# Optimization experiments

Measured on AMD Instinct MI355X. Metric: run time of the kernel, lower is better.

## Reference

```python
import jax, jax.numpy as jnp
import numpy as np

B, T, HID = 2, 1024, 4096
H, D_NOPE, D_ROPE, D_V = 32, 128, 64, 128
D_QK = D_NOPE + D_ROPE  # 192
Q_RANK, KV_RANK = 1536, 512
THETA, EPS = 10000.0, 1e-6
SCALE = D_QK ** -0.5
NEG = -1e30


def rms_norm(x, w):
    return x * jax.lax.rsqrt(jnp.mean(x * x, axis=-1, keepdims=True) + EPS) * w


def apply_rope(x, positions):
    # x: [B, T, h, d] (d even), positions: [B, T]
    d = x.shape[-1]
    inv_freq = 1.0 / (THETA ** (jnp.arange(0, d, 2, dtype=jnp.float32) / d))
    ang = positions.astype(jnp.float32)[:, :, None, None] * inv_freq  # [B,T,1,d/2]
    cos, sin = jnp.cos(ang), jnp.sin(ang)
    x1, x2 = jnp.split(x, 2, axis=-1)
    return jnp.concatenate([x1 * cos - x2 * sin, x1 * sin + x2 * cos], axis=-1)


def setup_inputs() -> dict:
    key = jax.random.key(0)
    ks = jax.random.split(key, 8)
    def lin(k, fan_in, fan_out):
        return (jax.random.normal(k, (fan_in, fan_out), jnp.float32)
                / np.float32(np.sqrt(fan_in)))
    return {
        "x": jax.random.normal(ks[0], (B, T, HID), jnp.float32),
        "wq_a": lin(ks[1], HID, Q_RANK),
        "q_norm_w": jnp.ones((Q_RANK,), jnp.float32),
        "wq_b": lin(ks[2], Q_RANK, H * D_QK),
        "wkv_a": lin(ks[3], HID, KV_RANK + D_ROPE),
        "kv_norm_w": jnp.ones((KV_RANK,), jnp.float32),
        "wkv_b": lin(ks[4], KV_RANK, H * (D_NOPE + D_V)),
        "wo": lin(ks[5], H * D_V, HID),
        "attention_mask": jnp.ones((B, T), jnp.int32),
        "positions": jnp.broadcast_to(jnp.arange(T, dtype=jnp.int32), (B, T)),
    }


def reference(x, wq_a, q_norm_w, wq_b, wkv_a, kv_norm_w, wkv_b, wo,
              attention_mask, positions):
    # ---- query path: low-rank down-proj, RMSNorm, up-proj ----
    q = rms_norm(x @ wq_a, q_norm_w) @ wq_b           # [B,T,H*D_QK]
    q = q.reshape(B, T, H, D_QK)
    q_nope, q_pe = jnp.split(q, [D_NOPE], axis=-1)
    q_pe = apply_rope(q_pe, positions)                # [B,T,H,D_ROPE]

    # ---- kv path: compressed latent + shared rope key ----
    kv_out = x @ wkv_a                                # [B,T,KV_RANK+D_ROPE]
    kv, k_pe = jnp.split(kv_out, [KV_RANK], axis=-1)
    k_pe = apply_rope(k_pe[:, :, None, :], positions) # [B,T,1,D_ROPE]
    kv_exp = rms_norm(kv, kv_norm_w) @ wkv_b          # [B,T,H*(D_NOPE+D_V)]
    kv_exp = kv_exp.reshape(B, T, H, D_NOPE + D_V)
    k_nope, v = jnp.split(kv_exp, [D_NOPE], axis=-1)

    q = jnp.concatenate([q_nope, q_pe], axis=-1)      # [B,T,H,D_QK]
    k = jnp.concatenate(
        [k_nope, jnp.broadcast_to(k_pe, (B, T, H, D_ROPE))], axis=-1)

    # ---- attention (causal + padding mask) ----
    scores = jnp.einsum('bthd,bshd->bhts', q, k) * SCALE     # [B,H,T,T]
    causal = jnp.tril(jnp.ones((T, T), dtype=bool))
    mask = causal[None, None] & (attention_mask[:, None, None, :] != 0)
    scores = jnp.where(mask, scores, NEG)
    attn = jax.nn.softmax(scores, axis=-1)
    out = jnp.einsum('bhts,bshd->bthd', attn, v)              # [B,T,H,D_V]
    return out.reshape(B, T, H * D_V) @ wo                    # [B,T,HID]
```

## Files before the change

kernel.cpp:

```cpp
#include <hip/hip_runtime.h>
#include <hip/hip_bf16.h>

#define BB 2
#define TT 1024
#define HIDD 4096
#define NH 32
#define DN 128
#define DR 64
#define DVV 128
#define DQK 192
#define QR 1536
#define KVR 512
#define MTOK (BB*TT)
#define EPSF 1e-6f
#define SCALEF 0.07216878364870322f

typedef unsigned short u16;
using bfrag = __attribute__((ext_vector_type(8))) short;
using f4 = __attribute__((ext_vector_type(4))) float;

__device__ __forceinline__ float bf2f(u16 u){
    union { unsigned int i; float f; } v; v.i = ((unsigned int)u) << 16; return v.f;
}
__device__ __forceinline__ u16 f2bf(float f){
    union { float f; unsigned int i; } v; v.f = f;
    unsigned int r = v.i + 0x7fffu + ((v.i >> 16) & 1u);
    return (u16)(r >> 16);
}
__device__ __forceinline__ void async16(const void* g, void* l){
    __builtin_amdgcn_global_load_lds((const __attribute__((address_space(1))) void*)g,
                                     (__attribute__((address_space(3))) void*)l, 16, 0, 0);
}

__global__ __launch_bounds__(256) void cvt_k(const float* __restrict__ in,
                                             u16* __restrict__ out, int n)
{
    int i = (blockIdx.x * 256 + threadIdx.x) * 4;
    if (i >= n) return;
    float4 v = *(const float4*)(in + i);
    ushort4 o = make_ushort4(f2bf(v.x), f2bf(v.y), f2bf(v.z), f2bf(v.w));
    *(ushort4*)(out + i) = o;
}

__global__ __launch_bounds__(256) void transpose_cvt(
    const float* __restrict__ W, u16* __restrict__ Wt, int Kd, int Nd)
{
    __shared__ u16 S[32][33];
    const int n0 = blockIdx.x * 32, k0 = blockIdx.y * 32;
    const int tx = threadIdx.x & 31, ty = threadIdx.x >> 5;
    #pragma unroll
    for (int i = 0; i < 4; ++i)
        S[ty + 8 * i][tx] = f2bf(W[(size_t)(k0 + ty + 8 * i) * Nd + n0 + tx]);
    __syncthreads();
    #pragma unroll
    for (int i = 0; i < 4; ++i)
        Wt[(size_t)(n0 + ty + 8 * i) * Kd + k0 + tx] = S[tx][ty + 8 * i];
}

template<int BN, int CMODE>
__global__ __launch_bounds__(256) void gemm_bt(
    const u16* __restrict__ A, const u16* __restrict__ Bt, void* __restrict__ C,
    u16* __restrict__ C2, int M, int N, int K, int lda)
{
    constexpr int BM = 128, BK = 32;
    constexpr int WAVES_N = (BN == 128) ? 2 : 1;
    constexpr int WAVES_M = 4 / WAVES_N;
    constexpr int WM = BM / WAVES_M, WN = BN / WAVES_N;
    constexpr int FM = WM / 16, FN = WN / 16;
    constexpr int RPWB = BN / 4;
    __shared__ alignas(16) u16 As[BM * BK];
    __shared__ alignas(16) u16 Bs[BN * BK];
    const int tid = threadIdx.x, w = tid >> 6, ln = tid & 63;
    const int row0 = blockIdx.y * BM, col0 = blockIdx.x * BN;
    const int wm = w / WAVES_N, wn = w % WAVES_N;
    const int lr = ln & 15, lq = ln >> 4;

    f4 acc[FM][FN];
    #pragma unroll
    for (int i = 0; i < FM; ++i)
        #pragma unroll
        for (int j = 0; j < FN; ++j)
            acc[i][j] = (f4){0.f, 0.f, 0.f, 0.f};

    const u16* gA = A + (size_t)(row0 + w * 32 + (ln >> 2)) * lda + (ln & 3) * 8;
    const u16* gB = Bt + (size_t)(col0 + w * RPWB + (ln >> 2)) * K + (ln & 3) * 8;

    for (int k0 = 0; k0 < K; k0 += BK) {
        #pragma unroll
        for (int i = 0; i < 2; ++i)
            async16(gA + (size_t)i * 16 * lda + k0, &As[(w * 32 + i * 16) * BK]);
        #pragma unroll
        for (int i = 0; i < RPWB / 16; ++i)
            async16(gB + (size_t)i * 16 * K + k0, &Bs[(w * RPWB + i * 16) * BK]);
        __syncthreads();
        bfrag af[FM], bf[FN];
        #pragma unroll
        for (int fm = 0; fm < FM; ++fm)
            af[fm] = *(const bfrag*)&As[(wm * WM + fm * 16 + lr) * BK + lq * 8];
        #pragma unroll
        for (int fn = 0; fn < FN; ++fn)
            bf[fn] = *(const bfrag*)&Bs[(wn * WN + fn * 16 + lr) * BK + lq * 8];
        #pragma unroll
        for (int fm = 0; fm < FM; ++fm)
            #pragma unroll
            for (int fn = 0; fn < FN; ++fn)
                acc[fm][fn] = __builtin_amdgcn_mfma_f32_16x16x32_bf16(
                    af[fm], bf[fn], acc[fm][fn], 0, 0, 0);
        __syncthreads();
    }
    #pragma unroll
    for (int fm = 0; fm < FM; ++fm)
        #pragma unroll
        for (int fn = 0; fn < FN; ++fn) {
            const int col = col0 + wn * WN + fn * 16 + lr;
            const int rowb = row0 + wm * WM + fm * 16 + lq * 4;
            if (CMODE == 2) {
                const int head = col >> 8, within = col & 255;
                if (within < DN) {
                    #pragma unroll
                    for (int r = 0; r < 4; ++r)
                        ((u16*)C)[(size_t)(rowb + r) * (NH * DN) + head * DN + within]
                            = f2bf(acc[fm][fn][r]);
                } else {
                    ushort4 pk = make_ushort4(f2bf(acc[fm][fn][0]), f2bf(acc[fm][fn][1]),
                                              f2bf(acc[fm][fn][2]), f2bf(acc[fm][fn][3]));
                    size_t off = ((size_t)((rowb >> 10) * NH + head) * DVV + (within - DN)) * TT
                                 + (rowb & (TT - 1));
                    *(ushort4*)(C2 + off) = pk;
                }
            } else {
                #pragma unroll
                for (int r = 0; r < 4; ++r) {
                    size_t off = (size_t)(rowb + r) * N + col;
                    if (CMODE == 1) ((float*)C)[off] = acc[fm][fn][r];
                    else            ((u16*)C)[off] = f2bf(acc[fm][fn][r]);
                }
            }
        }
}

__global__ __launch_bounds__(256) void rmsnorm_bf(
    u16* __restrict__ p, const float* __restrict__ w, int W, int stride)
{
    u16* x = p + (size_t)blockIdx.x * stride;
    __shared__ float red[256];
    float s = 0.f;
    for (int c = threadIdx.x; c < W; c += 256) { float v = bf2f(x[c]); s += v * v; }
    red[threadIdx.x] = s;
    __syncthreads();
    for (int off = 128; off > 0; off >>= 1) {
        if (threadIdx.x < off) red[threadIdx.x] += red[threadIdx.x + off];
        __syncthreads();
    }
    float scale = rsqrtf(red[0] / (float)W + EPSF);
    for (int c = threadIdx.x; c < W; c += 256)
        x[c] = f2bf(bf2f(x[c]) * scale * w[c]);
}

__global__ void rope_q_k(u16* __restrict__ q, const int* __restrict__ pos)
{
    int idx = blockIdx.x * 256 + threadIdx.x;
    if (idx >= MTOK * NH * 32) return;
    int j = idx & 31, h = (idx >> 5) & 31, tok = idx >> 10;
    u16* p = q + (size_t)tok * (NH * DQK) + h * DQK + DN;
    float x1 = bf2f(p[j]), x2 = bf2f(p[j + 32]);
    float inv = __expf((float)j * -0.28782313662425572f);
    float ang = (float)pos[tok] * inv;
    float sn, cs; sincosf(ang, &sn, &cs);
    p[j] = f2bf(x1 * cs - x2 * sn);
    p[j + 32] = f2bf(x1 * sn + x2 * cs);
}

__global__ void rope_k_k(const u16* __restrict__ kvd, u16* __restrict__ kpe,
                         const int* __restrict__ pos)
{
    int idx = blockIdx.x * 256 + threadIdx.x;
    if (idx >= MTOK * 32) return;
    int j = idx & 31, tok = idx >> 5;
    const u16* p = kvd + (size_t)tok * 576 + KVR;
    float x1 = bf2f(p[j]), x2 = bf2f(p[j + 32]);
    float inv = __expf((float)j * -0.28782313662425572f);
    float ang = (float)pos[tok] * inv;
    float sn, cs; sincosf(ang, &sn, &cs);
    kpe[(size_t)tok * 64 + j] = f2bf(x1 * cs - x2 * sn);
    kpe[(size_t)tok * 64 + j + 32] = f2bf(x1 * sn + x2 * cs);
}

struct SMa {
    alignas(16) u16 Ks[2][64 * 192];
    alignas(16) u16 Ps[4][16 * 72];
};
struct SMb { alignas(16) u16 Ot[64 * 136]; };
union SMu { SMa a; SMb o; };

__global__ __launch_bounds__(256, 2) void attn_mfma(
    const u16* __restrict__ q, const u16* __restrict__ KN,
    const u16* __restrict__ kpe, const u16* __restrict__ VT,
    const int* __restrict__ amask, u16* __restrict__ O)
{
    __shared__ SMu sm;
    const int tid = threadIdx.x, w = tid >> 6, ln = tid & 63;
    const int lr = ln & 15, lq = ln >> 4;
    const int h = blockIdx.x, b = blockIdx.z;
    const u16* vtb = VT + (size_t)(b * NH + h) * DVV * TT;

    auto stage = [&](u16* dst, int k0) {
        #pragma unroll
        for (int i = 0; i < 6; ++i) {
            const int p = (w * 6 + i) * 64 + ln;
            const int row = p / 24;
            const int c = (p - row * 24) ^ (row & 7);
            const int col = c << 3;
            const u16* src = (col < DN)
                ? KN + (size_t)(b * TT + k0 + row) * (NH * DN) + h * DN + col
                : kpe + (size_t)(b * TT + k0 + row) * 64 + (col - DN);
            async16(src, dst + (w * 6 + i) * 512);
        }
    };

    #pragma unroll
    for (int pass = 0; pass < 2; ++pass) {
        const int t = pass ? (15 - blockIdx.y) : blockIdx.y;
        const int q0 = t * 64;
        const int qg0 = q0 + w * 16 + lq * 4;

        bfrag qf[6];
        const u16* qbase = q + (size_t)(b * TT + q0 + w * 16 + lr) * (NH * DQK) + h * DQK + lq * 8;
        #pragma unroll
        for (int ks = 0; ks < 6; ++ks) qf[ks] = *(const bfrag*)(qbase + ks * 32);

        f4 acc[8];
        #pragma unroll
        for (int i = 0; i < 8; ++i) acc[i] = (f4){0.f, 0.f, 0.f, 0.f};
        float m_i[4], l_i[4];
        #pragma unroll
        for (int r = 0; r < 4; ++r) { m_i[r] = -1e30f; l_i[r] = 0.f; }

        __syncthreads();
        stage(sm.a.Ks[0], 0);
        __syncthreads();

        u16* cur = sm.a.Ks[0];
        u16* nxt = sm.a.Ks[1];
        const int nkt = t + 1;
        for (int kt = 0; kt < nkt; ++kt) {
            const int k0 = kt * 64;

            float mb[4];
            #pragma unroll
            for (int nt = 0; nt < 4; ++nt)
                mb[nt] = amask[b * TT + k0 + nt * 16 + lr] ? 0.f : -1e30f;
            bfrag vf0[8], vf1[8];
            #pragma unroll
            for (int d = 0; d < 8; ++d) {
                const u16* vrow = vtb + (size_t)(d * 16 + lr) * TT + k0 + lq * 8;
                vf0[d] = *(const bfrag*)vrow;
                vf1[d] = *(const bfrag*)(vrow + 32);
            }
            if (kt + 1 < nkt) stage(nxt, k0 + 64);

            f4 sacc[4];
            #pragma unroll
            for (int nt = 0; nt < 4; ++nt) {
                sacc[nt] = (f4){0.f, 0.f, 0.f, 0.f};
                const int r_ = nt * 16 + lr;
                const u16* kr = cur + r_ * 192;
                const int sw = r_ & 7;
                #pragma unroll
                for (int ks = 0; ks < 6; ++ks) {
                    bfrag kf = *(const bfrag*)(kr + (((ks * 4 + lq) ^ sw) << 3));
                    sacc[nt] = __builtin_amdgcn_mfma_f32_16x16x32_bf16(qf[ks], kf, sacc[nt], 0, 0, 0);
                }
            }

            float s[4][4];
            #pragma unroll
            for (int nt = 0; nt < 4; ++nt) {
                const int keyg = k0 + nt * 16 + lr;
                #pragma unroll
                for (int r = 0; r < 4; ++r) {
                    float v = sacc[nt][r] * SCALEF + mb[nt];
                    s[nt][r] = (keyg <= qg0 + r) ? v : -1e30f;
                }
            }
            #pragma unroll
            for (int r = 0; r < 4; ++r) {
                float tm = fmaxf(fmaxf(s[0][r], s[1][r]), fmaxf(s[2][r], s[3][r]));
                tm = fmaxf(tm, __shfl_xor(tm, 1));
                tm = fmaxf(tm, __shfl_xor(tm, 2));
                tm = fmaxf(tm, __shfl_xor(tm, 4));
                tm = fmaxf(tm, __shfl_xor(tm, 8));
                float m_new = fmaxf(m_i[r], tm);
                float alpha = __expf(m_i[r] - m_new);
                float p0 = __expf(s[0][r] - m_new);
                float p1 = __expf(s[1][r] - m_new);
                float p2 = __expf(s[2][r] - m_new);
                float p3 = __expf(s[3][r] - m_new);
                float rs = (p0 + p1) + (p2 + p3);
                rs += __shfl_xor(rs, 1);
                rs += __shfl_xor(rs, 2);
                rs += __shfl_xor(rs, 4);
                rs += __shfl_xor(rs, 8);
                l_i[r] = l_i[r] * alpha + rs;
                m_i[r] = m_new;
                #pragma unroll
                for (int d = 0; d < 8; ++d) acc[d][r] *= alpha;
                sm.a.Ps[w][(lq * 4 + r) * 72 + lr] = f2bf(p0);
                sm.a.Ps[w][(lq * 4 + r) * 72 + 16 + lr] = f2bf(p1);
                sm.a.Ps[w][(lq * 4 + r) * 72 + 32 + lr] = f2bf(p2);
                sm.a.Ps[w][(lq * 4 + r) * 72 + 48 + lr] = f2bf(p3);
            }
            bfrag pf0 = *(const bfrag*)&sm.a.Ps[w][lr * 72 + lq * 8];
            bfrag pf1 = *(const bfrag*)&sm.a.Ps[w][lr * 72 + 32 + lq * 8];
            #pragma unroll
            for (int d = 0; d < 8; ++d) {
                acc[d] = __builtin_amdgcn_mfma_f32_16x16x32_bf16(pf0, vf0[d], acc[d], 0, 0, 0);
                acc[d] = __builtin_amdgcn_mfma_f32_16x16x32_bf16(pf1, vf1[d], acc[d], 0, 0, 0);
            }
            __syncthreads();
            u16* tmp = cur; cur = nxt; nxt = tmp;
        }
        float inv_l[4];
        #pragma unroll
        for (int r = 0; r < 4; ++r) inv_l[r] = 1.0f / l_i[r];
        #pragma unroll
        for (int d = 0; d < 8; ++d)
            #pragma unroll
            for (int r = 0; r < 4; ++r)
                sm.o.Ot[(w * 16 + lq * 4 + r) * 136 + d * 16 + lr] = f2bf(acc[d][r] * inv_l[r]);
        __syncthreads();
        #pragma unroll
        for (int it = 0; it < 8; ++it) {
            int u = it * 256 + tid;
            int orow = u >> 5, ocol = (u & 31) * 4;
            ushort4 o4 = *(const ushort4*)&sm.o.Ot[orow * 136 + ocol];
            *(ushort4*)&O[(size_t)(b * TT + q0 + orow) * (NH * DVV) + h * DVV + ocol] = o4;
        }
    }
}

extern "C" void kernel_launch(void* const* d_in, const int* in_sizes, int n_in,
                              void* d_out, int out_size, void* d_ws, size_t ws_size,
                              hipStream_t stream)
{
    const float* x      = (const float*)d_in[0];
    const float* wq_a   = (const float*)d_in[1];
    const float* q_nw   = (const float*)d_in[2];
    const float* wq_b   = (const float*)d_in[3];
    const float* wkv_a  = (const float*)d_in[4];
    const float* kv_nw  = (const float*)d_in[5];
    const float* wkv_b  = (const float*)d_in[6];
    const float* wo     = (const float*)d_in[7];
    const int* amask    = (const int*)d_in[8];
    const int* pos      = (const int*)d_in[9];

    u16* ws = (u16*)d_ws;
    u16* wqa_t  = ws;
    u16* wqb_t  = wqa_t  + (size_t)QR * HIDD;
    u16* wkva_t = wqb_t  + (size_t)NH * DQK * QR;
    u16* wkvb_t = wkva_t + (size_t)576 * HIDD;
    u16* wo_t   = wkvb_t + (size_t)NH * 256 * KVR;
    u16* xb     = wo_t   + (size_t)HIDD * HIDD;
    u16* q_down = xb     + (size_t)MTOK * HIDD;
    u16* qbuf   = q_down + (size_t)MTOK * QR;
    u16* kvd    = qbuf   + (size_t)MTOK * NH * DQK;
    u16* kpe    = kvd    + (size_t)MTOK * 576;
    u16* KN     = kpe    + (size_t)MTOK * 64;
    u16* VT     = KN     + (size_t)MTOK * NH * DN;
    u16* Obuf   = wqa_t;

    cvt_k<<<(MTOK*HIDD/4 + 255)/256, 256, 0, stream>>>(x, xb, MTOK*HIDD);
    transpose_cvt<<<dim3(QR/32, HIDD/32), 256, 0, stream>>>(wq_a, wqa_t, HIDD, QR);
    transpose_cvt<<<dim3(NH*DQK/32, QR/32), 256, 0, stream>>>(wq_b, wqb_t, QR, NH*DQK);
    transpose_cvt<<<dim3(576/32, HIDD/32), 256, 0, stream>>>(wkv_a, wkva_t, HIDD, 576);
    transpose_cvt<<<dim3(NH*256/32, KVR/32), 256, 0, stream>>>(wkv_b, wkvb_t, KVR, NH*256);
    transpose_cvt<<<dim3(HIDD/32, HIDD/32), 256, 0, stream>>>(wo, wo_t, HIDD, HIDD);

    gemm_bt<128, 0><<<dim3(QR/128, MTOK/128), 256, 0, stream>>>(
        xb, wqa_t, q_down, nullptr, MTOK, QR, HIDD, HIDD);
    gemm_bt<64, 0><<<dim3(576/64, MTOK/128), 256, 0, stream>>>(
        xb, wkva_t, kvd, nullptr, MTOK, 576, HIDD, HIDD);
    rmsnorm_bf<<<MTOK, 256, 0, stream>>>(q_down, q_nw, QR, QR);
    rmsnorm_bf<<<MTOK, 256, 0, stream>>>(kvd, kv_nw, KVR, 576);
    rope_k_k<<<(MTOK*32 + 255)/256, 256, 0, stream>>>(kvd, kpe, pos);
    gemm_bt<128, 0><<<dim3(NH*DQK/128, MTOK/128), 256, 0, stream>>>(
        q_down, wqb_t, qbuf, nullptr, MTOK, NH*DQK, QR, QR);
    gemm_bt<128, 2><<<dim3(NH*256/128, MTOK/128), 256, 0, stream>>>(
        kvd, wkvb_t, KN, VT, MTOK, NH*256, KVR, 576);
    rope_q_k<<<(MTOK*NH*32 + 255)/256, 256, 0, stream>>>(qbuf, pos);
    attn_mfma<<<dim3(NH, 8, BB), 256, 0, stream>>>(qbuf, KN, kpe, VT, amask, Obuf);
    gemm_bt<128, 1><<<dim3(HIDD/128, MTOK/128), 256, 0, stream>>>(
        Obuf, wo_t, (float*)d_out, nullptr, MTOK, HIDD, NH*DVV, NH*DVV);
}
```

Measured before the change: 658.9 us.

## Double-buffer GEMM LDS tiles with BK=64 and XOR-swizzled layout

Reworks the bf16 GEMM main loop to use two LDS buffers, prefetching the next K tile asynchronously while MFMAs run on the current one. The K tile doubles to 64 and the shared-memory layout gets an XOR swizzle to cut bank conflicts on fragment reads. This drops one barrier per iteration and overlaps load latency with compute. In exchange it uses four times the LDS per block, which may lower occupancy.

```diff
diff --git a/kernel.cpp b/kernel.cpp
--- a/kernel.cpp
+++ b/kernel.cpp
@@ -62,18 +62,20 @@
     const u16* __restrict__ A, const u16* __restrict__ Bt, void* __restrict__ C,
     u16* __restrict__ C2, int M, int N, int K, int lda)
 {
-    constexpr int BM = 128, BK = 32;
+    constexpr int BM = 128, BK = 64;
     constexpr int WAVES_N = (BN == 128) ? 2 : 1;
     constexpr int WAVES_M = 4 / WAVES_N;
     constexpr int WM = BM / WAVES_M, WN = BN / WAVES_N;
     constexpr int FM = WM / 16, FN = WN / 16;
-    constexpr int RPWB = BN / 4;
-    __shared__ alignas(16) u16 As[BM * BK];
-    __shared__ alignas(16) u16 Bs[BN * BK];
+    constexpr int AISS = (BM * BK / 8) / 256;
+    constexpr int BISS = (BN * BK / 8) / 256;
+    __shared__ alignas(16) u16 As[2][BM * BK];
+    __shared__ alignas(16) u16 Bs[2][BN * BK];
     const int tid = threadIdx.x, w = tid >> 6, ln = tid & 63;
     const int row0 = blockIdx.y * BM, col0 = blockIdx.x * BN;
     const int wm = w / WAVES_N, wn = w % WAVES_N;
     const int lr = ln & 15, lq = ln >> 4;
+    const int sw = lr & 7;
 
     f4 acc[FM][FN];
     #pragma unroll
@@ -82,31 +84,48 @@
         for (int j = 0; j < FN; ++j)
             acc[i][j] = (f4){0.f, 0.f, 0.f, 0.f};
 
-    const u16* gA = A + (size_t)(row0 + w * 32 + (ln >> 2)) * lda + (ln & 3) * 8;
-    const u16* gB = Bt + (size_t)(col0 + w * RPWB + (ln >> 2)) * K + (ln & 3) * 8;
-
-    for (int k0 = 0; k0 < K; k0 += BK) {
-        #pragma unroll
-        for (int i = 0; i < 2; ++i)
-            async16(gA + (size_t)i * 16 * lda + k0, &As[(w * 32 + i * 16) * BK]);
-        #pragma unroll
-        for (int i = 0; i < RPWB / 16; ++i)
-            async16(gB + (size_t)i * 16 * K + k0, &Bs[(w * RPWB + i * 16) * BK]);
+    const int srow = ln >> 3;
+    const int scol = ((ln & 7) ^ srow) * 8;
+    const u16* pA = A + (size_t)(row0 + w * (AISS * 8) + srow) * lda + scol;
+    const u16* pB = Bt + (size_t)(col0 + w * (BISS * 8) + srow) * K + scol;
+
+    auto stageA = [&](int buf, int k0) {
+        #pragma unroll
+        for (int i = 0; i < AISS; ++i)
+            async16(pA + (size_t)i * 8 * lda + k0, &As[buf][(w * AISS + i) * 512]);
+    };
+    auto stageB = [&](int buf, int k0) {
+        #pragma unroll
+        for (int i = 0; i < BISS; ++i)
+            async16(pB + (size_t)i * 8 * K + k0, &Bs[buf][(w * BISS + i) * 512]);
+    };
+
+    stageA(0, 0); stageB(0, 0);
+    __syncthreads();
+
+    const int nkt = K / BK;
+    int cur = 0;
+    for (int kt = 0; kt < nkt; ++kt) {
+        if (kt + 1 < nkt) { stageA(cur ^ 1, (kt + 1) * BK); stageB(cur ^ 1, (kt + 1) * BK); }
+        #pragma unroll
+        for (int ks = 0; ks < 2; ++ks) {
+            const int sl = ((ks * 4 + lq) ^ sw) * 8;
+            bfrag af[FM], bfr[FN];
+            #pragma unroll
+            for (int fm = 0; fm < FM; ++fm)
+                af[fm] = *(const bfrag*)&As[cur][(wm * WM + fm * 16 + lr) * BK + sl];
+            #pragma unroll
+            for (int fn = 0; fn < FN; ++fn)
+                bfr[fn] = *(const bfrag*)&Bs[cur][(wn * WN + fn * 16 + lr) * BK + sl];
+            #pragma unroll
+            for (int fm = 0; fm < FM; ++fm)
+                #pragma unroll
+                for (int fn = 0; fn < FN; ++fn)
+                    acc[fm][fn] = __builtin_amdgcn_mfma_f32_16x16x32_bf16(
+                        af[fm], bfr[fn], acc[fm][fn], 0, 0, 0);
+        }
         __syncthreads();
-        bfrag af[FM], bf[FN];
-        #pragma unroll
-        for (int fm = 0; fm < FM; ++fm)
-            af[fm] = *(const bfrag*)&As[(wm * WM + fm * 16 + lr) * BK + lq * 8];
-        #pragma unroll
-        for (int fn = 0; fn < FN; ++fn)
-            bf[fn] = *(const bfrag*)&Bs[(wn * WN + fn * 16 + lr) * BK + lq * 8];
-        #pragma unroll
-        for (int fm = 0; fm < FM; ++fm)
-            #pragma unroll
-            for (int fn = 0; fn < FN; ++fn)
-                acc[fm][fn] = __builtin_amdgcn_mfma_f32_16x16x32_bf16(
-                    af[fm], bf[fn], acc[fm][fn], 0, 0, 0);
-        __syncthreads();
+        cur ^= 1;
     }
     #pragma unroll
     for (int fm = 0; fm < FM; ++fm)
```

New measurement: 586.2 us. 11.0% less time.
